# Kernel optimization log

Measured on AMD Instinct MI355X. Metric: run time of the kernel, lower is better.

The kernel has to match this reference:

```python
import jax, jax.numpy as jnp
import numpy as np

B, N, C, H, W = 256, 50000, 3, 32, 32


def setup_inputs() -> dict:
    key = jax.random.key(0)
    k1, k2, k3 = jax.random.split(key, 3)
    inp = jax.random.normal(k1, (B, C, H, W), dtype=jnp.float32)
    train_data = jax.random.normal(k2, (N, C, H, W), dtype=jnp.float32)
    # per-query noise levels in a realistic diffusion range
    sigma = jax.random.uniform(k3, (B,), dtype=jnp.float32) * 1.5 + 0.5
    return {"input": inp, "sigma": sigma, "train_data": train_data}


def reference(input, sigma, train_data):
    """Karras optimal denoiser:
    D(x, sigma) = sum_i y_i * Gau(x; y_i, sigma^2 I) / sum_i Gau(x; y_i, sigma^2 I).
    The Gaussian normalization constant (sigma*sqrt(2*pi))^D cancels in the ratio,
    so this is exactly softmax over -0.5*||x - y_i||^2 / sigma^2 (same math as the
    per-dim product of densities in the original, computed stably in log space).
    """
    b = input.shape[0]
    x = input.reshape(b, -1)                      # [B, D]
    y = train_data.reshape(train_data.shape[0], -1)  # [N, D]
    x2 = jnp.sum(x * x, axis=1, keepdims=True)    # [B, 1]
    y2 = jnp.sum(y * y, axis=1)                   # [N]
    # pairwise squared distances via GEMM: [B, N]
    sqdist = x2 + y2[None, :] - 2.0 * (x @ y.T)
    logw = -0.5 * sqdist / (sigma[:, None] ** 2)  # [B, N]
    w = jax.nn.softmax(logw, axis=1)              # normalized Gaussian weights
    out = w @ y                                   # [B, D] weighted average
    return out.reshape(input.shape)
```

## Files before the change

### kernel.cpp

```cpp
#include <hip/hip_runtime.h>
#include <hip/hip_bf16.h>
#include <type_traits>

#define BQ   256
#define NTR  50000
#define DD   3072
#define NSP  50048
#define NBLK 782
#define CAP  4096
#define DELTA 18.0f

typedef __fp16 f16;
typedef __fp16 f16x2 __attribute__((ext_vector_type(2)));
typedef __fp16 f16x8 __attribute__((ext_vector_type(8)));
typedef float  f32x4 __attribute__((ext_vector_type(4)));

__global__ __launch_bounds__(256) void kx(const float* __restrict__ x, f16* __restrict__ xp) {
    const int t = blockIdx.x * 256 + threadIdx.x;
    const int g = t >> 8, r = t & 255;
    const f32x4* src = (const f32x4*)(x + (size_t)r * DD + (g << 3));
    f32x4 a = src[0], b = src[1];
    union { f16x2 h2[4]; f16x8 h8; } u;
    u.h2[0] = __builtin_amdgcn_cvt_pkrtz(a[0], a[1]);
    u.h2[1] = __builtin_amdgcn_cvt_pkrtz(a[2], a[3]);
    u.h2[2] = __builtin_amdgcn_cvt_pkrtz(b[0], b[1]);
    u.h2[3] = __builtin_amdgcn_cvt_pkrtz(b[2], b[3]);
    ((f16x8*)xp)[t] = u.h8;
}

__global__ __launch_bounds__(512, 4) void kqk(
    const f16* __restrict__ xp, const float* __restrict__ y,
    float* __restrict__ S, float* __restrict__ pmax) {
    __shared__ char Bs[2][8192];

    const int tid = threadIdx.x;
    const int blk = blockIdx.x;
    const int n0  = blk * 64;

    const int ry   = tid >> 3;
    const int kp   = (tid & 7) << 3;
    const int yrow = n0 + ry;
    const bool yval = yrow < NTR;
    const float* ybase = y + (size_t)yrow * DD + kp;
    const int bo = ry * 128 + ((((tid & 7) << 4)) ^ ((ry & 7) << 4));

    const int w = tid >> 6, l = tid & 63;
    const int l15 = l & 15, lg = l >> 4;

    f32x4 acc[2][4] = {};
    float y2a = 0.f;
    f32x4 p0, p1, q0, q1;

    auto loady = [&](f32x4& a0, f32x4& a1, int ks) {
        if (yval) {
            const f32x4* pp = (const f32x4*)(ybase + (ks << 6));
            a0 = pp[0]; a1 = pp[1];
        } else { a0 = 0.f; a1 = 0.f; }
    };
    auto cvtw = [&](f32x4& a0, f32x4& a1, int buf) {
        y2a += a0[0]*a0[0] + a0[1]*a0[1] + a0[2]*a0[2] + a0[3]*a0[3]
             + a1[0]*a1[0] + a1[1]*a1[1] + a1[2]*a1[2] + a1[3]*a1[3];
        union { f16x2 h2[4]; f16x8 h8; } u;
        u.h2[0] = __builtin_amdgcn_cvt_pkrtz(a0[0], a0[1]);
        u.h2[1] = __builtin_amdgcn_cvt_pkrtz(a0[2], a0[3]);
        u.h2[2] = __builtin_amdgcn_cvt_pkrtz(a1[0], a1[1]);
        u.h2[3] = __builtin_amdgcn_cvt_pkrtz(a1[2], a1[3]);
        *(f16x8*)(&Bs[buf][bo]) = u.h8;
    };

    loady(p0, p1, 0);
    loady(q0, q1, 1);
    cvtw(p0, p1, 0);
    asm volatile("s_waitcnt lgkmcnt(0)" ::: "memory");
    __builtin_amdgcn_s_barrier();

    const f16x8* ap = (const f16x8*)xp;
    const int arow = (w << 5) + l15;

    auto iter = [&](int ks, auto curC,
                    f32x4& s0, f32x4& s1,
                    f32x4& t0, f32x4& t1) {
        constexpr int cur = decltype(curC)::value;
        f16x8 af[2][2];
        #pragma unroll
        for (int kk = 0; kk < 2; ++kk)
            #pragma unroll
            for (int fm = 0; fm < 2; ++fm)
                af[kk][fm] = ap[(size_t)((ks << 3) + (kk << 2) + lg) * 256 + arow + (fm << 4)];
        if (ks + 2 < 48) loady(s0, s1, ks + 2);
        f16x8 bf[2][4];
        #pragma unroll
        for (int kk = 0; kk < 2; ++kk)
            #pragma unroll
            for (int fn = 0; fn < 4; ++fn) {
                int r = (fn << 4) + l15;
                bf[kk][fn] = *(const f16x8*)(&Bs[cur][r * 128 + (((kk << 6) + (lg << 4)) ^ ((r & 7) << 4))]);
            }
        #pragma unroll
        for (int kk = 0; kk < 2; ++kk)
            #pragma unroll
            for (int fm = 0; fm < 2; ++fm)
                #pragma unroll
                for (int fn = 0; fn < 4; ++fn)
                    acc[fm][fn] = __builtin_amdgcn_mfma_f32_16x16x32_f16(af[kk][fm], bf[kk][fn], acc[fm][fn], 0, 0, 0);
        if (ks + 1 < 48) cvtw(t0, t1, cur ^ 1);
        asm volatile("s_waitcnt lgkmcnt(0)" ::: "memory");
        __builtin_amdgcn_s_barrier();
    };

    for (int ks2 = 0; ks2 < 48; ks2 += 2) {
        iter(ks2,     std::integral_constant<int,0>{}, p0, p1, q0, q1);
        iter(ks2 + 1, std::integral_constant<int,1>{}, q0, q1, p0, p1);
    }

    float* lys = (float*)&Bs[0][0];
    y2a += __shfl_xor(y2a, 1, 64);
    y2a += __shfl_xor(y2a, 2, 64);
    y2a += __shfl_xor(y2a, 4, 64);
    if ((tid & 7) == 0) lys[ry] = y2a;
    __syncthreads();
    float ly2[4];
    #pragma unroll
    for (int fn = 0; fn < 4; ++fn) ly2[fn] = 0.5f * lys[(fn << 4) + l15];
    #pragma unroll
    for (int fm = 0; fm < 2; ++fm) {
        #pragma unroll
        for (int j = 0; j < 4; ++j) {
            float rm = -3.4e38f;
            #pragma unroll
            for (int fn = 0; fn < 4; ++fn) {
                int col = n0 + (fn << 4) + l15;
                float sc = acc[fm][fn][j] - ly2[fn];
                rm = (col < NTR) ? fmaxf(rm, sc) : rm;
            }
            #pragma unroll
            for (int off = 1; off < 16; off <<= 1) rm = fmaxf(rm, __shfl_xor(rm, off, 64));
            if (l15 == 0)
                pmax[(size_t)((w << 5) + (fm << 4) + (lg << 2) + j) * NBLK + blk] = rm;
        }
    }
    #pragma unroll
    for (int fm = 0; fm < 2; ++fm) {
        int row0 = (w << 5) + (fm << 4) + (lg << 2);
        #pragma unroll
        for (int fn = 0; fn < 4; ++fn) {
            int col = n0 + (fn << 4) + l15;
            float* sp = S + (size_t)row0 * NSP + col;
            sp[0]               = acc[fm][fn][0] - ly2[fn];
            sp[NSP]             = acc[fm][fn][1] - ly2[fn];
            sp[2 * (size_t)NSP] = acc[fm][fn][2] - ly2[fn];
            sp[3 * (size_t)NSP] = acc[fm][fn][3] - ly2[fn];
        }
    }
}

__global__ __launch_bounds__(256) void ksel(
    const float* __restrict__ S, const float* __restrict__ pmax,
    const float* __restrict__ sig, unsigned* __restrict__ cnt,
    unsigned* __restrict__ cand) {
    __shared__ float red[4];
    const int b = blockIdx.x, tid = threadIdx.x;
    const float s2 = sig[b] * sig[b];
    const float* pm = pmax + (size_t)b * NBLK;
    float mx = -3.4e38f;
    for (int i = tid; i < NBLK; i += 256) mx = fmaxf(mx, pm[i]);
    #pragma unroll
    for (int o = 1; o < 64; o <<= 1) mx = fmaxf(mx, __shfl_xor(mx, o, 64));
    if ((tid & 63) == 0) red[tid >> 6] = mx;
    __syncthreads();
    mx = fmaxf(fmaxf(red[0], red[1]), fmaxf(red[2], red[3]));
    const float thr = mx - DELTA * s2;
    const f32x4* rowv = (const f32x4*)(S + (size_t)b * NSP);
    for (int i = tid; i < 12500; i += 256) {
        f32x4 s = rowv[i];
        #pragma unroll
        for (int j = 0; j < 4; ++j) {
            if (s[j] >= thr) {
                unsigned idx = atomicAdd(&cnt[b], 1u);
                if (idx < CAP) cand[(size_t)b * CAP + idx] = (unsigned)(4 * i + j);
            }
        }
    }
}

__global__ __launch_bounds__(512) void kpv(
    const float* __restrict__ x, const float* __restrict__ y,
    const float* __restrict__ sig, const unsigned* __restrict__ cnt,
    const unsigned* __restrict__ cand, float* __restrict__ out) {
    __shared__ float xs[DD];
    __shared__ unsigned ci[CAP];
    __shared__ float om[8], ol[8];
    __shared__ float sumv[DD];
    const int b = blockIdx.x, tid = threadIdx.x;
    const int c = (int)(cnt[b] < (unsigned)CAP ? cnt[b] : (unsigned)CAP);
    const float s2 = sig[b] * sig[b];
    const float isc = -0.5f / s2;
    for (int i = tid; i < DD; i += 512) xs[i] = x[(size_t)b * DD + i];
    for (int i = tid; i < c; i += 512) ci[i] = cand[(size_t)b * CAP + i];
    __syncthreads();
    const int w = tid >> 6, l = tid & 63;
    const f32x4* xr = (const f32x4*)xs;

    f32x4 o[12] = {};
    float m = -3.4e38f, ll = 0.f;
    f32x4 A[12], Bv[12];

    auto LD = [&](f32x4* dst, int i) {
        const f32x4* yr = (const f32x4*)(y + (size_t)ci[i] * DD);
        #pragma unroll
        for (int j = 0; j < 12; ++j) dst[j] = yr[(j << 6) + l];
    };
    auto PROC = [&](f32x4* src) {
        float d2 = 0.f;
        #pragma unroll
        for (int j = 0; j < 12; ++j) {
            f32x4 xv = xr[(j << 6) + l];
            float a0 = xv[0]-src[j][0], a1 = xv[1]-src[j][1],
                  a2 = xv[2]-src[j][2], a3 = xv[3]-src[j][3];
            d2 += a0*a0 + a1*a1 + a2*a2 + a3*a3;
        }
        #pragma unroll
        for (int off = 1; off < 64; off <<= 1) d2 += __shfl_xor(d2, off, 64);
        float s = d2 * isc;
        float mn = fmaxf(m, s);
        float f = __expf(m - mn);
        float wi = __expf(s - mn);
        #pragma unroll
        for (int j = 0; j < 12; ++j) o[j] = o[j] * f + wi * src[j];
        ll = ll * f + wi;
        m = mn;
    };

    int i = w;
    if (i < c) LD(A, i);
    for (; i < c; i += 16) {
        int i2 = i + 8;
        if (i2 < c) LD(Bv, i2);
        PROC(A);
        if (i2 < c) {
            if (i + 16 < c) LD(A, i + 16);
            PROC(Bv);
        }
    }
    om[w] = m; ol[w] = ll;
    __syncthreads();
    float M = om[0];
    #pragma unroll
    for (int ww = 1; ww < 8; ++ww) M = fmaxf(M, om[ww]);
    float Ls = 0.f;
    #pragma unroll
    for (int ww = 0; ww < 8; ++ww) Ls += ol[ww] * __expf(om[ww] - M);
    const float fw = __expf(m - M);
    f32x4* sv = (f32x4*)sumv;
    if (w == 0) {
        #pragma unroll
        for (int j = 0; j < 12; ++j) sv[(j << 6) + l] = o[j] * fw;
    }
    __syncthreads();
    for (int ww = 1; ww < 8; ++ww) {
        if (w == ww) {
            #pragma unroll
            for (int j = 0; j < 12; ++j) sv[(j << 6) + l] += o[j] * fw;
        }
        __syncthreads();
    }
    const float inv = 1.f / Ls;
    f32x4* od = (f32x4*)(out + (size_t)b * DD);
    for (int t = tid; t < 768; t += 512) od[t] = sv[t] * inv;
}

extern "C" void kernel_launch(void* const* d_in, const int* in_sizes, int n_in,
                              void* d_out, int out_size, void* d_ws, size_t ws_size,
                              hipStream_t stream) {
    const float* x   = (const float*)d_in[0];
    const float* sig = (const float*)d_in[1];
    const float* y   = (const float*)d_in[2];
    float* out = (float*)d_out;
    char* ws = (char*)d_ws;
    f16*      xp   = (f16*)(ws);
    unsigned* cnt  = (unsigned*)(ws + 1572864);
    unsigned* cand = (unsigned*)(ws + 1573888);
    float*    pmax = (float*)(ws + 5768192);
    float*    S    = (float*)(ws + 6568960);

    (void)hipMemsetAsync(cnt, 0, 256 * sizeof(unsigned), stream);
    kx  <<<384, 256, 0, stream>>>(x, xp);
    kqk <<<NBLK, 512, 0, stream>>>(xp, y, S, pmax);
    ksel<<<256, 256, 0, stream>>>(S, pmax, sig, cnt, cand);
    kpv <<<256, 512, 0, stream>>>(x, y, sig, cnt, cand, out);
}
```

Measured before the change: 280.9 us.

## Stage fp32 train rows into LDS via direct global-to-LDS loads with wider K tiles

The QK kernel now copies fp32 train-data tiles straight from global memory into LDS with global_load_lds. It no longer loads them into registers, converts them to fp16 and stores them back. Each stage covers 256 K elements (12 stages instead of 48), so there are fewer barriers. The fp32-to-fp16 conversion and the y^2 norm accumulation move to the LDS read side, with only warp 0 computing norms. The cost is a 128KB LDS footprint, which lowers occupancy to 2 blocks, and every warp repeats the conversion work.

```diff
diff --git a/kernel.cpp b/kernel.cpp
--- a/kernel.cpp
+++ b/kernel.cpp
@@ -14,6 +14,12 @@
 typedef __fp16 f16x2 __attribute__((ext_vector_type(2)));
 typedef __fp16 f16x8 __attribute__((ext_vector_type(8)));
 typedef float  f32x4 __attribute__((ext_vector_type(4)));
+
+__device__ __forceinline__ void gload_lds16(const void* g, void* l) {
+    __builtin_amdgcn_global_load_lds(
+        (const __attribute__((address_space(1))) unsigned int*)g,
+        (__attribute__((address_space(3))) unsigned int*)l, 16, 0, 0);
+}
 
 __global__ __launch_bounds__(256) void kx(const float* __restrict__ x, f16* __restrict__ xp) {
     const int t = blockIdx.x * 256 + threadIdx.x;
@@ -28,96 +34,93 @@
     ((f16x8*)xp)[t] = u.h8;
 }
 
-__global__ __launch_bounds__(512, 4) void kqk(
+__global__ __launch_bounds__(512, 2) void kqk(
     const f16* __restrict__ xp, const float* __restrict__ y,
     float* __restrict__ S, float* __restrict__ pmax) {
-    __shared__ char Bs[2][8192];
+    __shared__ char Bs[2][65536];
 
     const int tid = threadIdx.x;
     const int blk = blockIdx.x;
     const int n0  = blk * 64;
-
-    const int ry   = tid >> 3;
-    const int kp   = (tid & 7) << 3;
-    const int yrow = n0 + ry;
-    const bool yval = yrow < NTR;
-    const float* ybase = y + (size_t)yrow * DD + kp;
-    const int bo = ry * 128 + ((((tid & 7) << 4)) ^ ((ry & 7) << 4));
-
     const int w = tid >> 6, l = tid & 63;
     const int l15 = l & 15, lg = l >> 4;
 
-    f32x4 acc[2][4] = {};
-    float y2a = 0.f;
-    f32x4 p0, p1, q0, q1;
-
-    auto loady = [&](f32x4& a0, f32x4& a1, int ks) {
-        if (yval) {
-            const f32x4* pp = (const f32x4*)(ybase + (ks << 6));
-            a0 = pp[0]; a1 = pp[1];
-        } else { a0 = 0.f; a1 = 0.f; }
+    const char* ysrc[8];
+    #pragma unroll
+    for (int j = 0; j < 8; ++j) {
+        int row  = n0 + (w << 3) + j;
+        int rowc = row < NTR ? row : NTR - 1;
+        ysrc[j] = (const char*)(y + (size_t)rowc * DD) + (((l << 4) ^ (j << 4)));
+    }
+
+    auto stage = [&](int buf, int ks) {
+        #pragma unroll
+        for (int j = 0; j < 8; ++j)
+            gload_lds16(ysrc[j] + (ks << 10), &Bs[buf][(((w << 3) + j) << 10)]);
     };
-    auto cvtw = [&](f32x4& a0, f32x4& a1, int buf) {
-        y2a += a0[0]*a0[0] + a0[1]*a0[1] + a0[2]*a0[2] + a0[3]*a0[3]
-             + a1[0]*a1[0] + a1[1]*a1[1] + a1[2]*a1[2] + a1[3]*a1[3];
-        union { f16x2 h2[4]; f16x8 h8; } u;
-        u.h2[0] = __builtin_amdgcn_cvt_pkrtz(a0[0], a0[1]);
-        u.h2[1] = __builtin_amdgcn_cvt_pkrtz(a0[2], a0[3]);
-        u.h2[2] = __builtin_amdgcn_cvt_pkrtz(a1[0], a1[1]);
-        u.h2[3] = __builtin_amdgcn_cvt_pkrtz(a1[2], a1[3]);
-        *(f16x8*)(&Bs[buf][bo]) = u.h8;
-    };
-
-    loady(p0, p1, 0);
-    loady(q0, q1, 1);
-    cvtw(p0, p1, 0);
-    asm volatile("s_waitcnt lgkmcnt(0)" ::: "memory");
-    __builtin_amdgcn_s_barrier();
+
+    stage(0, 0);
+    __syncthreads();
 
     const f16x8* ap = (const f16x8*)xp;
     const int arow = (w << 5) + l15;
-
-    auto iter = [&](int ks, auto curC,
-                    f32x4& s0, f32x4& s1,
-                    f32x4& t0, f32x4& t1) {
-        constexpr int cur = decltype(curC)::value;
-        f16x8 af[2][2];
-        #pragma unroll
-        for (int kk = 0; kk < 2; ++kk)
+    f32x4 acc[2][4] = {};
+    float y2a[4] = {0.f, 0.f, 0.f, 0.f};
+
+    for (int ks = 0; ks < 12; ++ks) {
+        const int cur = ks & 1;
+        f16x8 af[8][2];
+        #pragma unroll
+        for (int kk = 0; kk < 8; ++kk)
             #pragma unroll
             for (int fm = 0; fm < 2; ++fm)
-                af[kk][fm] = ap[(size_t)((ks << 3) + (kk << 2) + lg) * 256 + arow + (fm << 4)];
-        if (ks + 2 < 48) loady(s0, s1, ks + 2);
-        f16x8 bf[2][4];
-        #pragma unroll
-        for (int kk = 0; kk < 2; ++kk)
+                af[kk][fm] = ap[(size_t)((ks << 5) + (kk << 2) + lg) * 256 + arow + (fm << 4)];
+        __builtin_amdgcn_sched_barrier(0);
+        if (ks < 11) stage(cur ^ 1, ks + 1);
+        __builtin_amdgcn_sched_barrier(0);
+        const char* Bc = Bs[cur];
+        #pragma unroll
+        for (int kk = 0; kk < 8; ++kk) {
+            f16x8 bf[4];
             #pragma unroll
             for (int fn = 0; fn < 4; ++fn) {
-                int r = (fn << 4) + l15;
-                bf[kk][fn] = *(const f16x8*)(&Bs[cur][r * 128 + (((kk << 6) + (lg << 4)) ^ ((r & 7) << 4))]);
+                const int r = (fn << 4) + l15;
+                const int m = (r & 7) << 4;
+                const int p = (kk << 7) + (lg << 5);
+                f32x4 lo = *(const f32x4*)(Bc + (r << 10) + (p ^ m));
+                f32x4 hi = *(const f32x4*)(Bc + (r << 10) + ((p + 16) ^ m));
+                if (w == 0) {
+                    y2a[fn] += lo[0]*lo[0] + lo[1]*lo[1] + lo[2]*lo[2] + lo[3]*lo[3]
+                             + hi[0]*hi[0] + hi[1]*hi[1] + hi[2]*hi[2] + hi[3]*hi[3];
+                }
+                union { f16x2 h2[4]; f16x8 h8; } u;
+                u.h2[0] = __builtin_amdgcn_cvt_pkrtz(lo[0], lo[1]);
+                u.h2[1] = __builtin_amdgcn_cvt_pkrtz(lo[2], lo[3]);
+                u.h2[2] = __builtin_amdgcn_cvt_pkrtz(hi[0], hi[1]);
+                u.h2[3] = __builtin_amdgcn_cvt_pkrtz(hi[2], hi[3]);
+                bf[fn] = u.h8;
             }
-        #pragma unroll
-        for (int kk = 0; kk < 2; ++kk)
             #pragma unroll
             for (int fm = 0; fm < 2; ++fm)
                 #pragma unroll
                 for (int fn = 0; fn < 4; ++fn)
-                    acc[fm][fn] = __builtin_amdgcn_mfma_f32_16x16x32_f16(af[kk][fm], bf[kk][fn], acc[fm][fn], 0, 0, 0);
-        if (ks + 1 < 48) cvtw(t0, t1, cur ^ 1);
-        asm volatile("s_waitcnt lgkmcnt(0)" ::: "memory");
-        __builtin_amdgcn_s_barrier();
-    };
-
-    for (int ks2 = 0; ks2 < 48; ks2 += 2) {
-        iter(ks2,     std::integral_constant<int,0>{}, p0, p1, q0, q1);
-        iter(ks2 + 1, std::integral_constant<int,1>{}, q0, q1, p0, p1);
+                    acc[fm][fn] = __builtin_amdgcn_mfma_f32_16x16x32_f16(af[kk][fm], bf[fn], acc[fm][fn], 0, 0, 0);
+        }
+        __syncthreads();
     }
 
     float* lys = (float*)&Bs[0][0];
-    y2a += __shfl_xor(y2a, 1, 64);
-    y2a += __shfl_xor(y2a, 2, 64);
-    y2a += __shfl_xor(y2a, 4, 64);
-    if ((tid & 7) == 0) lys[ry] = y2a;
+    #pragma unroll
+    for (int fn = 0; fn < 4; ++fn) {
+        float v = y2a[fn];
+        v += __shfl_xor(v, 16, 64);
+        v += __shfl_xor(v, 32, 64);
+        y2a[fn] = v;
+    }
+    if (w == 0 && lg == 0) {
+        #pragma unroll
+        for (int fn = 0; fn < 4; ++fn) lys[(fn << 4) + l15] = y2a[fn];
+    }
     __syncthreads();
     float ly2[4];
     #pragma unroll
```

Measured after the change: 332.9 us. 18.5% more time.

## Store score matrix in fp16 and fuse candidate selection into weighted-sum kernel

Applied to the files above, without the earlier changes.

The score matrix S is now written as fp16 instead of fp32, which halves the large intermediate write and read. The separate selection kernel, its global atomic counter and memset are removed; the PV kernel now computes the row max, scans the fp16 scores and collects candidates into shared memory with shared atomics. The threshold gets an extra margin to cover fp16 rounding, which may admit more candidates and risks hitting the CAP limit. The fp16 scores are used only for selection, while exact distances are recomputed in fp32.

```diff
diff --git a/kernel.cpp b/kernel.cpp
--- a/kernel.cpp
+++ b/kernel.cpp
@@ -30,7 +30,7 @@
 
 __global__ __launch_bounds__(512, 4) void kqk(
     const f16* __restrict__ xp, const float* __restrict__ y,
-    float* __restrict__ S, float* __restrict__ pmax) {
+    f16* __restrict__ S, float* __restrict__ pmax) {
     __shared__ char Bs[2][8192];
 
     const int tid = threadIdx.x;
@@ -145,62 +145,60 @@
         #pragma unroll
         for (int fn = 0; fn < 4; ++fn) {
             int col = n0 + (fn << 4) + l15;
-            float* sp = S + (size_t)row0 * NSP + col;
-            sp[0]               = acc[fm][fn][0] - ly2[fn];
-            sp[NSP]             = acc[fm][fn][1] - ly2[fn];
-            sp[2 * (size_t)NSP] = acc[fm][fn][2] - ly2[fn];
-            sp[3 * (size_t)NSP] = acc[fm][fn][3] - ly2[fn];
-        }
-    }
-}
-
-__global__ __launch_bounds__(256) void ksel(
-    const float* __restrict__ S, const float* __restrict__ pmax,
-    const float* __restrict__ sig, unsigned* __restrict__ cnt,
-    unsigned* __restrict__ cand) {
-    __shared__ float red[4];
-    const int b = blockIdx.x, tid = threadIdx.x;
-    const float s2 = sig[b] * sig[b];
-    const float* pm = pmax + (size_t)b * NBLK;
-    float mx = -3.4e38f;
-    for (int i = tid; i < NBLK; i += 256) mx = fmaxf(mx, pm[i]);
-    #pragma unroll
-    for (int o = 1; o < 64; o <<= 1) mx = fmaxf(mx, __shfl_xor(mx, o, 64));
-    if ((tid & 63) == 0) red[tid >> 6] = mx;
-    __syncthreads();
-    mx = fmaxf(fmaxf(red[0], red[1]), fmaxf(red[2], red[3]));
-    const float thr = mx - DELTA * s2;
-    const f32x4* rowv = (const f32x4*)(S + (size_t)b * NSP);
-    for (int i = tid; i < 12500; i += 256) {
-        f32x4 s = rowv[i];
-        #pragma unroll
-        for (int j = 0; j < 4; ++j) {
-            if (s[j] >= thr) {
-                unsigned idx = atomicAdd(&cnt[b], 1u);
-                if (idx < CAP) cand[(size_t)b * CAP + idx] = (unsigned)(4 * i + j);
-            }
-        }
-    }
-}
-
-__global__ __launch_bounds__(512) void kpv(
+            f16* sp = S + (size_t)row0 * NSP + col;
+            sp[0]               = (f16)(acc[fm][fn][0] - ly2[fn]);
+            sp[NSP]             = (f16)(acc[fm][fn][1] - ly2[fn]);
+            sp[2 * (size_t)NSP] = (f16)(acc[fm][fn][2] - ly2[fn]);
+            sp[3 * (size_t)NSP] = (f16)(acc[fm][fn][3] - ly2[fn]);
+        }
+    }
+}
+
+__global__ __launch_bounds__(512) void ksp(
     const float* __restrict__ x, const float* __restrict__ y,
-    const float* __restrict__ sig, const unsigned* __restrict__ cnt,
-    const unsigned* __restrict__ cand, float* __restrict__ out) {
+    const f16* __restrict__ S, const float* __restrict__ pmax,
+    const float* __restrict__ sig, float* __restrict__ out) {
     __shared__ float xs[DD];
     __shared__ unsigned ci[CAP];
+    __shared__ unsigned scnt;
+    __shared__ float red[8];
     __shared__ float om[8], ol[8];
     __shared__ float sumv[DD];
     const int b = blockIdx.x, tid = threadIdx.x;
-    const int c = (int)(cnt[b] < (unsigned)CAP ? cnt[b] : (unsigned)CAP);
     const float s2 = sig[b] * sig[b];
     const float isc = -0.5f / s2;
+    const int w = tid >> 6, l = tid & 63;
+
+    if (tid == 0) scnt = 0;
     for (int i = tid; i < DD; i += 512) xs[i] = x[(size_t)b * DD + i];
-    for (int i = tid; i < c; i += 512) ci[i] = cand[(size_t)b * CAP + i];
-    __syncthreads();
-    const int w = tid >> 6, l = tid & 63;
+    const float* pm = pmax + (size_t)b * NBLK;
+    float mx = -3.4e38f;
+    for (int i = tid; i < NBLK; i += 512) mx = fmaxf(mx, pm[i]);
+    #pragma unroll
+    for (int o = 1; o < 64; o <<= 1) mx = fmaxf(mx, __shfl_xor(mx, o, 64));
+    if (l == 0) red[w] = mx;
+    __syncthreads();
+    mx = red[0];
+    #pragma unroll
+    for (int ww = 1; ww < 8; ++ww) mx = fmaxf(mx, red[ww]);
+    const float thr = mx - DELTA * s2 - 2.0f;
+
+    const f16x8* row = (const f16x8*)(S + (size_t)b * NSP);
+    for (int i = tid; i < 6256; i += 512) {
+        f16x8 v = row[i];
+        #pragma unroll
+        for (int j = 0; j < 8; ++j) {
+            int idx = (i << 3) + j;
+            if ((float)v[j] >= thr && idx < NTR) {
+                unsigned p = atomicAdd(&scnt, 1u);
+                if (p < CAP) ci[p] = (unsigned)idx;
+            }
+        }
+    }
+    __syncthreads();
+    const int c = (int)(scnt < (unsigned)CAP ? scnt : (unsigned)CAP);
+
     const f32x4* xr = (const f32x4*)xs;
-
     f32x4 o[12] = {};
     float m = -3.4e38f, ll = 0.f;
     f32x4 A[12], Bv[12];
@@ -277,15 +275,11 @@
     const float* y   = (const float*)d_in[2];
     float* out = (float*)d_out;
     char* ws = (char*)d_ws;
-    f16*      xp   = (f16*)(ws);
-    unsigned* cnt  = (unsigned*)(ws + 1572864);
-    unsigned* cand = (unsigned*)(ws + 1573888);
-    float*    pmax = (float*)(ws + 5768192);
-    float*    S    = (float*)(ws + 6568960);
-
-    (void)hipMemsetAsync(cnt, 0, 256 * sizeof(unsigned), stream);
+    f16*   xp   = (f16*)(ws);
+    float* pmax = (float*)(ws + 1572864);
+    f16*   S    = (f16*)(ws + 2373632);
+
     kx  <<<384, 256, 0, stream>>>(x, xp);
     kqk <<<NBLK, 512, 0, stream>>>(xp, y, S, pmax);
-    ksel<<<256, 256, 0, stream>>>(S, pmax, sig, cnt, cand);
-    kpv <<<256, 512, 0, stream>>>(x, y, sig, cnt, cand, out);
-}
+    ksp <<<256, 512, 0, stream>>>(x, y, S, pmax, sig, out);
+}
```

New measurement: 245.9 us. -12.5%, faster.
